# Kernel tuning notes

Hardware: AMD Instinct MI355X
Metric: run time of the kernel (lower is better)

The kernel has to match this reference:

```python
import jax, jax.numpy as jnp
import numpy as np

BATCH = 8192
IN_FEATURES = 4096
OUT_FEATURES = 4096
PACKED_LEN = (IN_FEATURES + 7) // 8  # 512


def _unpack_pm1(x_packed):
    """Unpack uint8-valued ints (stored as int32) into +/-1 float32, LSB-first.
    [.., P] -> [.., P*8]; bit 1 -> +1.0, bit 0 -> -1.0."""
    bits = (x_packed[..., None] >> jnp.arange(8, dtype=x_packed.dtype)) & 1
    bits = bits.reshape(*x_packed.shape[:-1], x_packed.shape[-1] * 8)
    return (2.0 * bits - 1.0).astype(jnp.float32)


def setup_inputs() -> dict:
    key = jax.random.key(0)
    k1, k2, k3 = jax.random.split(key, 3)
    input_packed = jax.random.randint(k1, (BATCH, PACKED_LEN), 0, 256, dtype=jnp.int32)
    weight_packed = jax.random.randint(k2, (OUT_FEATURES, PACKED_LEN), 0, 256, dtype=jnp.int32)
    bias = jax.random.normal(k3, (OUT_FEATURES,), dtype=jnp.float32) * 0.01
    return {"input_packed": input_packed, "weight_packed": weight_packed, "bias": bias}


def reference(input_packed, weight_packed, bias):
    # BitLinear: +/-1 dot product == in_features - 2*popcount(a XOR w)
    a = _unpack_pm1(input_packed)   # [B, in_features]
    w = _unpack_pm1(weight_packed)  # [out_features, in_features]
    out = jnp.einsum('bk,ok->bo', a, w)  # fp32 accumulate, [B, out_features]
    return out + bias
```

## Files before the change

### kernel.cpp

```cpp
#include <hip/hip_runtime.h>
#include <stdint.h>


typedef int v4i  __attribute__((ext_vector_type(4)));
typedef int v16i __attribute__((ext_vector_type(16)));

#define BATCH 8192
#define OUTF  4096
#define KDIM  4096
#define BM    256
#define BN    256
#define NPAIR 32

__device__ __forceinline__ uint32_t pack4(int4 q) {
    return (uint32_t)q.x | ((uint32_t)q.y << 8) |
           ((uint32_t)q.z << 16) | ((uint32_t)q.w << 24);
}

__global__ __launch_bounds__(256) void bitpack(const int* __restrict__ ap,
                                               const int* __restrict__ wp,
                                               uint4* __restrict__ Ab,
                                               uint4* __restrict__ Wb) {
    int t = blockIdx.x * 256 + threadIdx.x;
    const int* src;
    uint4* dst;
    if (t < BATCH * NPAIR) {
        const int p = t >> 13, m = t & 8191;
        src = ap + m * 512 + p * 16;
        dst = Ab + (p * BATCH + m);
    } else {
        const int u = t - BATCH * NPAIR;
        const int p = u >> 12, n = u & 4095;
        src = wp + n * 512 + p * 16;
        dst = Wb + (p * OUTF + n);
    }
    const int4* s4 = (const int4*)src;
    int4 q0 = s4[0], q1 = s4[1], q2 = s4[2], q3 = s4[3];
    uint4 o;
    o.x = pack4(q0); o.y = pack4(q1); o.z = pack4(q2); o.w = pack4(q3);
    *dst = o;
}

__device__ __forceinline__ uint32_t spread4(uint32_t n) {
    return (n * 0x204081u) & 0x01010101u;
}
__device__ __forceinline__ v4i expand16(uint32_t x) {
    v4i r;
    r[0] = (int)spread4(x & 0xFu);
    r[1] = (int)spread4((x >> 4) & 0xFu);
    r[2] = (int)spread4((x >> 8) & 0xFu);
    r[3] = (int)spread4(x >> 12);
    return r;
}

__global__ __launch_bounds__(512, 2) void bitgemm_fused(const v4i* __restrict__ Ab,
                                                        const v4i* __restrict__ Wb,
                                                        const float* __restrict__ bias,
                                                        float* __restrict__ out) {
    const int tid  = threadIdx.x;
    const int lane = tid & 63;
    const int w    = __builtin_amdgcn_readfirstlane(tid >> 6);
    const int wr   = w >> 2;
    const int wc   = w & 3;
    const int rl   = lane & 31;
    const int hl16 = (lane >> 5) * 16;
    const int bx   = blockIdx.x;
    const int by   = blockIdx.y;

    const int rowA0 = by * 256 + wr * 128 + rl;
    const int rowW0 = bx * 256 + wc * 64 + rl;

    v16i acc[4][2];
#pragma unroll
    for (int mt = 0; mt < 4; ++mt)
#pragma unroll
        for (int nt = 0; nt < 2; ++nt)
#pragma unroll
            for (int rg = 0; rg < 16; ++rg) acc[mt][nt][rg] = 0;

    int ars[4] = {0, 0, 0, 0};
    int wrs[2] = {0, 0};

    auto loadPair = [&](v4i (&pa)[4], v4i (&pw)[2], int p) {
#pragma unroll
        for (int mt = 0; mt < 4; ++mt)
            pa[mt] = Ab[(size_t)p * BATCH + rowA0 + mt * 32];
#pragma unroll
        for (int nt = 0; nt < 2; ++nt)
            pw[nt] = Wb[(size_t)p * OUTF + rowW0 + nt * 32];
    };

    auto computePair = [&](const v4i (&pa)[4], const v4i (&pw)[2]) {
#pragma unroll
        for (int mt = 0; mt < 4; ++mt)
            ars[mt] += __popc((uint32_t)pa[mt][0]) + __popc((uint32_t)pa[mt][1]) +
                       __popc((uint32_t)pa[mt][2]) + __popc((uint32_t)pa[mt][3]);
#pragma unroll
        for (int nt = 0; nt < 2; ++nt)
            wrs[nt] += __popc((uint32_t)pw[nt][0]) + __popc((uint32_t)pw[nt][1]) +
                       __popc((uint32_t)pw[nt][2]) + __popc((uint32_t)pw[nt][3]);
#pragma unroll
        for (int c = 0; c < 4; ++c) {
            v4i av[4], wv[2];
#pragma unroll
            for (int mt = 0; mt < 4; ++mt)
                av[mt] = expand16(((uint32_t)pa[mt][c] >> hl16) & 0xFFFFu);
#pragma unroll
            for (int nt = 0; nt < 2; ++nt)
                wv[nt] = expand16(((uint32_t)pw[nt][c] >> hl16) & 0xFFFFu);
            __builtin_amdgcn_s_setprio(1);
#pragma unroll
            for (int mt = 0; mt < 4; ++mt) {
                acc[mt][0] = __builtin_amdgcn_mfma_i32_32x32x32_i8(av[mt], wv[0],
                                                                   acc[mt][0], 0, 0, 0);
                acc[mt][1] = __builtin_amdgcn_mfma_i32_32x32x32_i8(av[mt], wv[1],
                                                                   acc[mt][1], 0, 0, 0);
            }
            __builtin_amdgcn_s_setprio(0);
        }
    };

    v4i pa0[4], pw0[2], pa1[4], pw1[2];
    loadPair(pa0, pw0, 0);
#pragma unroll 1
    for (int pp = 0; pp < NPAIR / 2; ++pp) {
        loadPair(pa1, pw1, 2 * pp + 1);
        computePair(pa0, pw0);
        if (pp < NPAIR / 2 - 1) loadPair(pa0, pw0, 2 * pp + 2);
        computePair(pa1, pw1);
    }

    const int cl = lane & 31;
    const int r0 = (lane >> 5) * 4;
    const int m0 = by * BM;
    const int n0 = bx * BN;
#pragma unroll
    for (int mt = 0; mt < 4; ++mt) {
#pragma unroll
        for (int nt = 0; nt < 2; ++nt) {
            const int col = n0 + (wc * 2 + nt) * 32 + cl;
            const float bv = bias[col];
            const int rw2 = 2 * wrs[nt];
#pragma unroll
            for (int rg = 0; rg < 16; ++rg) {
                const int rig = r0 + (rg & 3) + 8 * (rg >> 2);
                const int ra  = __shfl(ars[mt], rig);
                const int v   = 4 * acc[mt][nt][rg] - 2 * ra - rw2 + KDIM;
                const int row = m0 + (wr * 4 + mt) * 32 + rig;
                out[(size_t)row * OUTF + col] = (float)v + bv;
            }
        }
    }
}

extern "C" void kernel_launch(void* const* d_in, const int* in_sizes, int n_in,
                              void* d_out, int out_size, void* d_ws, size_t ws_size,
                              hipStream_t stream) {
    const int*   a_packed = (const int*)d_in[0];
    const int*   w_packed = (const int*)d_in[1];
    const float* bias     = (const float*)d_in[2];
    float*       out      = (float*)d_out;

    uint4* Ab = (uint4*)d_ws;
    uint4* Wb = (uint4*)((char*)d_ws + (size_t)BATCH * 512);

    const int total = (BATCH + OUTF) * NPAIR;
    bitpack<<<total / 256, 256, 0, stream>>>(a_packed, w_packed, Ab, Wb);

    dim3 grid(OUTF / BN, BATCH / BM);
    bitgemm_fused<<<grid, 512, 0, stream>>>((const v4i*)Ab, (const v4i*)Wb,
                                            bias, out);
}
```

Measured before the change: 259.2 us.

## Precompute row popcounts in pack kernel, use perm-based bit expansion, shrink GEMM tiles

Row popcounts of A and W are now computed once in the bitpack kernel via atomics and read in the epilogue, instead of being recomputed per block inside the GEMM loop. Bit expansion to int8 lanes uses byte-permute plus masks, with W bits byte-reversed at pack time so the expanded product places values at a fixed bit position; the accumulator is shifted right by 4 to recover the count. Block tiles shrink from 256x256 with 8 waves to 128x128 with 4 waves and target occupancy of 4 blocks per CU. This adds a memset, global atomics, and more global reloads of A/W per block because of the smaller tiles.

```diff
diff --git a/kernel.cpp b/kernel.cpp
--- a/kernel.cpp
+++ b/kernel.cpp
@@ -8,119 +8,131 @@
 #define BATCH 8192
 #define OUTF  4096
 #define KDIM  4096
-#define BM    256
-#define BN    256
 #define NPAIR 32
 
 __device__ __forceinline__ uint32_t pack4(int4 q) {
     return (uint32_t)q.x | ((uint32_t)q.y << 8) |
            ((uint32_t)q.z << 16) | ((uint32_t)q.w << 24);
 }
+__device__ __forceinline__ uint32_t bytebitrev(uint32_t x) {
+    return __builtin_bswap32(__brev(x));
+}
 
 __global__ __launch_bounds__(256) void bitpack(const int* __restrict__ ap,
                                                const int* __restrict__ wp,
                                                uint4* __restrict__ Ab,
-                                               uint4* __restrict__ Wb) {
+                                               uint4* __restrict__ Wb,
+                                               int* __restrict__ rsA,
+                                               int* __restrict__ rsW) {
     int t = blockIdx.x * 256 + threadIdx.x;
     const int* src;
     uint4* dst;
+    int* rs;
+    bool isW;
     if (t < BATCH * NPAIR) {
         const int p = t >> 13, m = t & 8191;
         src = ap + m * 512 + p * 16;
         dst = Ab + (p * BATCH + m);
+        rs  = rsA + m;
+        isW = false;
     } else {
         const int u = t - BATCH * NPAIR;
         const int p = u >> 12, n = u & 4095;
         src = wp + n * 512 + p * 16;
         dst = Wb + (p * OUTF + n);
+        rs  = rsW + n;
+        isW = true;
     }
     const int4* s4 = (const int4*)src;
     int4 q0 = s4[0], q1 = s4[1], q2 = s4[2], q3 = s4[3];
     uint4 o;
     o.x = pack4(q0); o.y = pack4(q1); o.z = pack4(q2); o.w = pack4(q3);
+    const int pc = __popc(o.x) + __popc(o.y) + __popc(o.z) + __popc(o.w);
+    atomicAdd(rs, pc);
+    if (isW) {
+        o.x = bytebitrev(o.x); o.y = bytebitrev(o.y);
+        o.z = bytebitrev(o.z); o.w = bytebitrev(o.w);
+    }
     *dst = o;
 }
 
-__device__ __forceinline__ uint32_t spread4(uint32_t n) {
-    return (n * 0x204081u) & 0x01010101u;
+__device__ __forceinline__ v4i expandA(uint32_t w, uint32_t s0, uint32_t s1) {
+    uint32_t p0 = __builtin_amdgcn_perm(w, w, s0);
+    uint32_t p1 = __builtin_amdgcn_perm(w, w, s1);
+    v4i r;
+    r[0] = (int)(p0 & 0x08040201u);
+    r[1] = (int)((p0 & 0x80402010u) >> 1);
+    r[2] = (int)(p1 & 0x08040201u);
+    r[3] = (int)((p1 & 0x80402010u) >> 1);
+    return r;
 }
-__device__ __forceinline__ v4i expand16(uint32_t x) {
+__device__ __forceinline__ v4i expandW(uint32_t w, uint32_t s0, uint32_t s1) {
+    uint32_t p0 = __builtin_amdgcn_perm(w, w, s0);
+    uint32_t p1 = __builtin_amdgcn_perm(w, w, s1);
     v4i r;
-    r[0] = (int)spread4(x & 0xFu);
-    r[1] = (int)spread4((x >> 4) & 0xFu);
-    r[2] = (int)spread4((x >> 8) & 0xFu);
-    r[3] = (int)spread4(x >> 12);
+    r[0] = (int)((p0 & 0x10204080u) >> 1);
+    r[1] = (int)(p0 & 0x01020408u);
+    r[2] = (int)((p1 & 0x10204080u) >> 1);
+    r[3] = (int)(p1 & 0x01020408u);
     return r;
 }
 
-__global__ __launch_bounds__(512, 2) void bitgemm_fused(const v4i* __restrict__ Ab,
+__global__ __launch_bounds__(256, 4) void bitgemm_fused(const v4i* __restrict__ Ab,
                                                         const v4i* __restrict__ Wb,
+                                                        const int* __restrict__ rsA,
+                                                        const int* __restrict__ rsW,
                                                         const float* __restrict__ bias,
                                                         float* __restrict__ out) {
     const int tid  = threadIdx.x;
     const int lane = tid & 63;
     const int w    = __builtin_amdgcn_readfirstlane(tid >> 6);
-    const int wr   = w >> 2;
-    const int wc   = w & 3;
+    const int wr   = w >> 1;
+    const int wc   = w & 1;
     const int rl   = lane & 31;
-    const int hl16 = (lane >> 5) * 16;
+    const int h    = lane >> 5;
     const int bx   = blockIdx.x;
     const int by   = blockIdx.y;
 
-    const int rowA0 = by * 256 + wr * 128 + rl;
-    const int rowW0 = bx * 256 + wc * 64 + rl;
+    const uint32_t s0 = h ? 0x02020202u : 0x00000000u;
+    const uint32_t s1 = s0 + 0x01010101u;
 
-    v16i acc[4][2];
+    const int rowA0 = by * 128 + wr * 64 + rl;
+    const int rowW0 = bx * 128 + wc * 64 + rl;
+
+    v16i acc[2][2];
 #pragma unroll
-    for (int mt = 0; mt < 4; ++mt)
+    for (int mt = 0; mt < 2; ++mt)
 #pragma unroll
         for (int nt = 0; nt < 2; ++nt)
 #pragma unroll
             for (int rg = 0; rg < 16; ++rg) acc[mt][nt][rg] = 0;
 
-    int ars[4] = {0, 0, 0, 0};
-    int wrs[2] = {0, 0};
-
-    auto loadPair = [&](v4i (&pa)[4], v4i (&pw)[2], int p) {
+    auto loadPair = [&](v4i (&pa)[2], v4i (&pw)[2], int p) {
 #pragma unroll
-        for (int mt = 0; mt < 4; ++mt)
+        for (int mt = 0; mt < 2; ++mt)
             pa[mt] = Ab[(size_t)p * BATCH + rowA0 + mt * 32];
 #pragma unroll
         for (int nt = 0; nt < 2; ++nt)
             pw[nt] = Wb[(size_t)p * OUTF + rowW0 + nt * 32];
     };
 
-    auto computePair = [&](const v4i (&pa)[4], const v4i (&pw)[2]) {
-#pragma unroll
-        for (int mt = 0; mt < 4; ++mt)
-            ars[mt] += __popc((uint32_t)pa[mt][0]) + __popc((uint32_t)pa[mt][1]) +
-                       __popc((uint32_t)pa[mt][2]) + __popc((uint32_t)pa[mt][3]);
-#pragma unroll
-        for (int nt = 0; nt < 2; ++nt)
-            wrs[nt] += __popc((uint32_t)pw[nt][0]) + __popc((uint32_t)pw[nt][1]) +
-                       __popc((uint32_t)pw[nt][2]) + __popc((uint32_t)pw[nt][3]);
+    auto computePair = [&](const v4i (&pa)[2], const v4i (&pw)[2]) {
 #pragma unroll
         for (int c = 0; c < 4; ++c) {
-            v4i av[4], wv[2];
-#pragma unroll
-            for (int mt = 0; mt < 4; ++mt)
-                av[mt] = expand16(((uint32_t)pa[mt][c] >> hl16) & 0xFFFFu);
-#pragma unroll
-            for (int nt = 0; nt < 2; ++nt)
-                wv[nt] = expand16(((uint32_t)pw[nt][c] >> hl16) & 0xFFFFu);
+            v4i a0 = expandA((uint32_t)pa[0][c], s0, s1);
+            v4i a1 = expandA((uint32_t)pa[1][c], s0, s1);
+            v4i w0 = expandW((uint32_t)pw[0][c], s0, s1);
+            v4i w1 = expandW((uint32_t)pw[1][c], s0, s1);
             __builtin_amdgcn_s_setprio(1);
-#pragma unroll
-            for (int mt = 0; mt < 4; ++mt) {
-                acc[mt][0] = __builtin_amdgcn_mfma_i32_32x32x32_i8(av[mt], wv[0],
-                                                                   acc[mt][0], 0, 0, 0);
-                acc[mt][1] = __builtin_amdgcn_mfma_i32_32x32x32_i8(av[mt], wv[1],
-                                                                   acc[mt][1], 0, 0, 0);
-            }
+            acc[0][0] = __builtin_amdgcn_mfma_i32_32x32x32_i8(a0, w0, acc[0][0], 0, 0, 0);
+            acc[0][1] = __builtin_amdgcn_mfma_i32_32x32x32_i8(a0, w1, acc[0][1], 0, 0, 0);
+            acc[1][0] = __builtin_amdgcn_mfma_i32_32x32x32_i8(a1, w0, acc[1][0], 0, 0, 0);
+            acc[1][1] = __builtin_amdgcn_mfma_i32_32x32x32_i8(a1, w1, acc[1][1], 0, 0, 0);
             __builtin_amdgcn_s_setprio(0);
         }
     };
 
-    v4i pa0[4], pw0[2], pa1[4], pw1[2];
+    v4i pa0[2], pw0[2], pa1[2], pw1[2];
     loadPair(pa0, pw0, 0);
 #pragma unroll 1
     for (int pp = 0; pp < NPAIR / 2; ++pp) {
@@ -132,21 +144,20 @@
 
     const int cl = lane & 31;
     const int r0 = (lane >> 5) * 4;
-    const int m0 = by * BM;
-    const int n0 = bx * BN;
+    const int m0 = by * 128 + wr * 64;
+    const int n0 = bx * 128 + wc * 64;
 #pragma unroll
-    for (int mt = 0; mt < 4; ++mt) {
+    for (int mt = 0; mt < 2; ++mt) {
 #pragma unroll
         for (int nt = 0; nt < 2; ++nt) {
-            const int col = n0 + (wc * 2 + nt) * 32 + cl;
+            const int col = n0 + nt * 32 + cl;
             const float bv = bias[col];
-            const int rw2 = 2 * wrs[nt];
+            const int rw2 = 2 * rsW[col];
 #pragma unroll
             for (int rg = 0; rg < 16; ++rg) {
                 const int rig = r0 + (rg & 3) + 8 * (rg >> 2);
-                const int ra  = __shfl(ars[mt], rig);
-                const int v   = 4 * acc[mt][nt][rg] - 2 * ra - rw2 + KDIM;
-                const int row = m0 + (wr * 4 + mt) * 32 + rig;
+                const int row = m0 + mt * 32 + rig;
+                const int v = (acc[mt][nt][rg] >> 4) - 2 * rsA[row] - rw2 + KDIM;
                 out[(size_t)row * OUTF + col] = (float)v + bv;
             }
         }
@@ -163,11 +174,15 @@
 
     uint4* Ab = (uint4*)d_ws;
     uint4* Wb = (uint4*)((char*)d_ws + (size_t)BATCH * 512);
+    int*   rsA = (int*)((char*)d_ws + 6u * 1024 * 1024);
+    int*   rsW = rsA + BATCH;
+
+    hipMemsetAsync(rsA, 0, (BATCH + OUTF) * sizeof(int), stream);
 
     const int total = (BATCH + OUTF) * NPAIR;
-    bitpack<<<total / 256, 256, 0, stream>>>(a_packed, w_packed, Ab, Wb);
+    bitpack<<<total / 256, 256, 0, stream>>>(a_packed, w_packed, Ab, Wb, rsA, rsW);
 
-    dim3 grid(OUTF / BN, BATCH / BM);
-    bitgemm_fused<<<grid, 512, 0, stream>>>((const v4i*)Ab, (const v4i*)Wb,
-                                            bias, out);
+    dim3 grid(OUTF / 128, BATCH / 128);
+    bitgemm_fused<<<grid, 256, 0, stream>>>((const v4i*)Ab, (const v4i*)Wb,
+                                            rsA, rsW, bias, out);
 }
```

Measured after the change: 250.3 us. 1.04x faster.
